# Optimization experiments

Measured on AMD Instinct MI355X. Metric: run time of the kernel, lower is better.

## Reference

```python
import math
import jax, jax.numpy as jnp
import numpy as np
from jax import lax

N_NODES = 325
D = 64
K = 12
E = 2600
SLOTS = 288
WEEK = 7
CHUNK = 24  # 2016 = 84 * 24; chunking does not change the math (disconnected copies)


def _mlp2(x, w1, b1, w2, b2):
    return jax.nn.relu(x @ w1 + b1) @ w2 + b2


def _gru_last_hidden(seq, w_ih, w_hh, b_ih, b_hh, hid):
    # seq: [N, K, 1]; torch nn.GRU gate equations, return final hidden [N, hid]
    def step(h, x_t):
        gi = x_t @ w_ih + b_ih            # [N, 3H]
        gh = h @ w_hh + b_hh
        i_r, i_z, i_n = jnp.split(gi, 3, axis=-1)
        h_r, h_z, h_n = jnp.split(gh, 3, axis=-1)
        r = jax.nn.sigmoid(i_r + h_r)
        z = jax.nn.sigmoid(i_z + h_z)
        n = jnp.tanh(i_n + r * h_n)
        return (1.0 - z) * n + z * h, None
    h0 = jnp.zeros((seq.shape[0], hid), seq.dtype)
    h, _ = lax.scan(step, h0, jnp.swapaxes(seq, 0, 1))  # scan over K
    return h


def _gat(x, src, dst, W, att_src, att_dst, bias, n_nodes):
    # PyG GATConv (self loops already appended to src/dst), concat=False -> head mean
    # x: [C, N, Din]; W: [Din, H*Dh]; att_*: [H, Dh]
    C = x.shape[0]
    H, Dh = att_src.shape
    xp = (x @ W).reshape(C, n_nodes, H, Dh)
    a_s = jnp.sum(xp * att_src, axis=-1)   # [C, N, H]
    a_d = jnp.sum(xp * att_dst, axis=-1)
    e = jax.nn.leaky_relu(a_s[:, src] + a_d[:, dst], 0.2)   # [C, Eb, H]
    seg_max = jax.vmap(lambda v: jax.ops.segment_max(v, dst, num_segments=n_nodes))(e)
    ex = jnp.exp(e - seg_max[:, dst])
    den = jax.vmap(lambda v: jax.ops.segment_sum(v, dst, num_segments=n_nodes))(ex)
    alpha = ex / (den[:, dst] + 1e-16)                       # softmax per dst node
    msg = xp[:, src] * alpha[..., None]                      # [C, Eb, H, Dh]
    out = jax.vmap(lambda m: jax.ops.segment_sum(m, dst, num_segments=n_nodes))(msg)
    return out.mean(axis=2) + bias                           # [C, N, Dh]


def setup_inputs() -> dict:
    key = jax.random.key(0)
    ks = iter(jax.random.split(key, 40))
    s = 0.05
    f = jnp.float32
    p = {}
    p["H_base_bank"] = jax.random.normal(next(ks), (WEEK, SLOTS, N_NODES, D), f)
    p["recent_speed_seq"] = jax.random.normal(next(ks), (N_NODES, K, 1), f)
    p["edge_index"] = jax.random.randint(next(ks), (2, E), 0, N_NODES, jnp.int64 if jax.config.jax_enable_x64 else jnp.int32)
    # GRU (input 1 -> hidden 32)
    p["gru_w_ih"] = jax.random.normal(next(ks), (1, 96), f) * s
    p["gru_w_hh"] = jax.random.normal(next(ks), (32, 96), f) * s
    p["gru_b_ih"] = jnp.zeros((96,), f)
    p["gru_b_hh"] = jnp.zeros((96,), f)
    # recent proj MLP 32->32->32
    p["rp_w1"] = jax.random.normal(next(ks), (32, 32), f) * s; p["rp_b1"] = jnp.zeros((32,), f)
    p["rp_w2"] = jax.random.normal(next(ks), (32, 32), f) * s; p["rp_b2"] = jnp.zeros((32,), f)
    # calendar
    p["weekday_emb"] = jax.random.normal(next(ks), (7, 8), f) * s
    p["slot_emb"] = jax.random.normal(next(ks), (288, 16), f) * s
    p["cal_w1"] = jax.random.normal(next(ks), (29, 32), f) * s; p["cal_b1"] = jnp.zeros((32,), f)
    p["cal_w2"] = jax.random.normal(next(ks), (32, 32), f) * s; p["cal_b2"] = jnp.zeros((32,), f)
    # delta / gate MLPs (fusion 128 -> 64)
    p["dm_w1"] = jax.random.normal(next(ks), (128, 64), f) * s; p["dm_b1"] = jnp.zeros((64,), f)
    p["dm_w2"] = jax.random.normal(next(ks), (64, 64), f) * s;  p["dm_b2"] = jnp.zeros((64,), f)
    p["gm_w"] = jax.random.normal(next(ks), (128, 64), f) * s;  p["gm_b"] = jnp.zeros((64,), f)
    # GATConv 1 (heads=2, concat=False) and 2 (heads=1)
    p["g1_w"] = jax.random.normal(next(ks), (64, 128), f) * s
    p["g1_att_src"] = jax.random.normal(next(ks), (2, 64), f) * s
    p["g1_att_dst"] = jax.random.normal(next(ks), (2, 64), f) * s
    p["g1_bias"] = jnp.zeros((64,), f)
    p["g2_w"] = jax.random.normal(next(ks), (64, 64), f) * s
    p["g2_att_src"] = jax.random.normal(next(ks), (1, 64), f) * s
    p["g2_att_dst"] = jax.random.normal(next(ks), (1, 64), f) * s
    p["g2_bias"] = jnp.zeros((64,), f)
    # speed head 64->32->1
    p["sh_w1"] = jax.random.normal(next(ks), (64, 32), f) * s; p["sh_b1"] = jnp.zeros((32,), f)
    p["sh_w2"] = jax.random.normal(next(ks), (32, 1), f) * s;  p["sh_b2"] = jnp.zeros((1,), f)
    return p


def reference(H_base_bank, recent_speed_seq, edge_index,
              gru_w_ih, gru_w_hh, gru_b_ih, gru_b_hh,
              rp_w1, rp_b1, rp_w2, rp_b2,
              weekday_emb, slot_emb, cal_w1, cal_b1, cal_w2, cal_b2,
              dm_w1, dm_b1, dm_w2, dm_b2, gm_w, gm_b,
              g1_w, g1_att_src, g1_att_dst, g1_bias,
              g2_w, g2_att_src, g2_att_dst, g2_bias,
              sh_w1, sh_b1, sh_w2, sh_b2):
    W_, S_, N, Dm = H_base_bank.shape
    # --- recent encoder ---
    h = _gru_last_hidden(recent_speed_seq, gru_w_ih, gru_w_hh, gru_b_ih, gru_b_hh, 32)
    recent_summary = _mlp2(h, rp_w1, rp_b1, rp_w2, rp_b2)          # [N, 32]
    # --- calendar encoder ---
    w_ids = jnp.repeat(jnp.arange(WEEK)[:, None], SLOTS, axis=1)    # [7, 288]
    s_ids = jnp.repeat(jnp.arange(SLOTS)[None, :], WEEK, axis=0)
    w_e = weekday_emb[w_ids]
    s_e = slot_emb[s_ids]
    ta = 2.0 * math.pi * s_ids.astype(jnp.float32) / 288.0
    wa = 2.0 * math.pi * w_ids.astype(jnp.float32) / 7.0
    cyc = jnp.stack([jnp.sin(ta), jnp.cos(ta), jnp.sin(wa), jnp.cos(wa)], axis=-1)
    wknd = (w_ids >= 5).astype(jnp.float32)[..., None]
    cal_feat = jnp.concatenate([w_e, s_e, cyc, wknd], axis=-1)      # [7, 288, 29]
    calendar_emb = _mlp2(cal_feat, cal_w1, cal_b1, cal_w2, cal_b2)  # [7, 288, 32]
    # --- fusion ---
    rec_x = jnp.broadcast_to(recent_summary[None, None], (W_, S_, N, 32))
    cal_x = jnp.broadcast_to(calendar_emb[:, :, None, :], (W_, S_, N, 32))
    fusion = jnp.concatenate([H_base_bank, rec_x, cal_x], axis=-1)  # [7, 288, N, 128]
    delta_raw = _mlp2(fusion, dm_w1, dm_b1, dm_w2, dm_b2)
    gate = jax.nn.sigmoid(fusion @ gm_w + gm_b)
    delta = delta_raw * gate                                         # [7, 288, N, D]
    # --- graph propagation (GATConv adds self loops by default) ---
    src = jnp.concatenate([edge_index[0], jnp.arange(N, dtype=edge_index.dtype)])
    dst = jnp.concatenate([edge_index[1], jnp.arange(N, dtype=edge_index.dtype)])
    G = W_ * S_
    flat = delta.reshape(G // CHUNK, CHUNK, N, Dm)
    def body(carry, chunk):
        x = jax.nn.relu(_gat(chunk, src, dst, g1_w, g1_att_src, g1_att_dst, g1_bias, N))
        x = jax.nn.relu(_gat(x, src, dst, g2_w, g2_att_src, g2_att_dst, g2_bias, N))
        return carry, x
    _, prop = lax.scan(body, None, flat)
    delta_recent_bank = prop.reshape(W_, S_, N, Dm)
    H_adapted_bank = H_base_bank + delta_recent_bank
    pred_speed_bank = (_mlp2(H_adapted_bank, sh_w1, sh_b1, sh_w2, sh_b2)).squeeze(-1)
    return delta_recent_bank, H_adapted_bank, pred_speed_bank
```

## Files before the change

kernel.cpp:

```cpp
#include <hip/hip_runtime.h>
#include <math.h>

#define N_NODES 325
#define GTOT    2016
#define NPOS    655200
#define NEDGE   2600
#define EBTOT   2925

static __device__ __forceinline__ float bf2f(unsigned short u) {
  union { unsigned int i; float f; } x; x.i = ((unsigned int)u) << 16; return x.f;
}
static __device__ __forceinline__ unsigned short f2bf(float v) {
  union { unsigned int i; float f; } x; x.f = v;
  unsigned int r = x.i + 0x7fffu + ((x.i >> 16) & 1u);
  return (unsigned short)(r >> 16);
}
static __device__ __forceinline__ float sigm(float v) { return 1.f / (1.f + __expf(-v)); }

__global__ void k_csr(const int* __restrict__ ei, int* __restrict__ rowp,
                      int* __restrict__ cols) {
  __shared__ int cnt[N_NODES];
  __shared__ int offs[N_NODES];
  const int tid = threadIdx.x;
  for (int i = tid; i < N_NODES; i += blockDim.x) cnt[i] = 0;
  __syncthreads();
  for (int e = tid; e < EBTOT; e += blockDim.x) {
    int dst = (e < NEDGE) ? ei[NEDGE + e] : (e - NEDGE);
    atomicAdd(&cnt[dst], 1);
  }
  __syncthreads();
  if (tid == 0) {
    int run = 0;
    for (int i = 0; i < N_NODES; ++i) { offs[i] = run; rowp[i] = run; run += cnt[i]; }
    rowp[N_NODES] = run;
  }
  __syncthreads();
  for (int e = tid; e < EBTOT; e += blockDim.x) {
    int src, dst;
    if (e < NEDGE) { src = ei[e]; dst = ei[NEDGE + e]; }
    else           { src = e - NEDGE; dst = src; }
    int pos = atomicAdd(&offs[dst], 1);
    cols[pos] = src;
  }
}

__global__ __launch_bounds__(256) void k_gru(
    const float* __restrict__ seq,
    const float* __restrict__ w_ih, const float* __restrict__ w_hh,
    const float* __restrict__ b_ih, const float* __restrict__ b_hh,
    const float* __restrict__ rw1, const float* __restrict__ rb1,
    const float* __restrict__ rw2, const float* __restrict__ rb2,
    float* __restrict__ recent) {
  __shared__ float h[8][33];
  __shared__ float h2[8][33];
  const int tid = threadIdx.x;
  const int ln = tid >> 5, j = tid & 31;
  const int n = blockIdx.x * 8 + ln;
  h[ln][j] = 0.f;
  __syncthreads();
  for (int t = 0; t < 12; ++t) {
    float x = (n < N_NODES) ? seq[n * 12 + t] : 0.f;
    float i_r = fmaf(x, w_ih[j],      b_ih[j]);
    float i_z = fmaf(x, w_ih[32 + j], b_ih[32 + j]);
    float i_n = fmaf(x, w_ih[64 + j], b_ih[64 + j]);
    float h_r = b_hh[j], h_z = b_hh[32 + j], h_n = b_hh[64 + j];
    #pragma unroll
    for (int k = 0; k < 32; ++k) {
      float hk = h[ln][k];
      h_r = fmaf(hk, w_hh[k * 96 + j],      h_r);
      h_z = fmaf(hk, w_hh[k * 96 + 32 + j], h_z);
      h_n = fmaf(hk, w_hh[k * 96 + 64 + j], h_n);
    }
    float r  = sigm(i_r + h_r);
    float z  = sigm(i_z + h_z);
    float nn = tanhf(fmaf(r, h_n, i_n));
    float hw = (1.f - z) * nn + z * h[ln][j];
    __syncthreads();
    h[ln][j] = hw;
    __syncthreads();
  }
  float a = rb1[j];
  #pragma unroll
  for (int k = 0; k < 32; ++k) a = fmaf(h[ln][k], rw1[k * 32 + j], a);
  h2[ln][j] = fmaxf(a, 0.f);
  __syncthreads();
  float o = rb2[j];
  #pragma unroll
  for (int k = 0; k < 32; ++k) o = fmaf(h2[ln][k], rw2[k * 32 + j], o);
  if (n < N_NODES) recent[n * 32 + j] = o;
}

__global__ __launch_bounds__(256) void k_cal(
    const float* __restrict__ wemb, const float* __restrict__ semb,
    const float* __restrict__ w1, const float* __restrict__ b1,
    const float* __restrict__ w2, const float* __restrict__ b2,
    float* __restrict__ cal) {
  __shared__ float feat[8][32];
  __shared__ float hid[8][33];
  const int tid = threadIdx.x;
  const int ln = tid >> 5, j = tid & 31;
  const int pos = blockIdx.x * 8 + ln;
  const int w = pos / 288, s = pos - w * 288;
  const float TWO_PI = 6.283185307179586f;
  float f = 0.f;
  if (j < 8)       f = wemb[w * 8 + j];
  else if (j < 24) f = semb[s * 16 + (j - 8)];
  else if (j == 24) f = sinf(TWO_PI * (float)s / 288.f);
  else if (j == 25) f = cosf(TWO_PI * (float)s / 288.f);
  else if (j == 26) f = sinf(TWO_PI * (float)w / 7.f);
  else if (j == 27) f = cosf(TWO_PI * (float)w / 7.f);
  else if (j == 28) f = (w >= 5) ? 1.f : 0.f;
  feat[ln][j] = f;
  __syncthreads();
  float a = b1[j];
  #pragma unroll
  for (int k = 0; k < 29; ++k) a = fmaf(feat[ln][k], w1[k * 32 + j], a);
  hid[ln][j] = fmaxf(a, 0.f);
  __syncthreads();
  float o = b2[j];
  #pragma unroll
  for (int k = 0; k < 32; ++k) o = fmaf(hid[ln][k], w2[k * 32 + j], o);
  if (pos < GTOT) cal[pos * 32 + j] = o;
}

__global__ __launch_bounds__(256, 2) void k_fusion(
    const float* __restrict__ Hb, const float* __restrict__ recent,
    const float* __restrict__ cal,
    const float* __restrict__ dw1, const float* __restrict__ db1,
    const float* __restrict__ dw2, const float* __restrict__ db2,
    const float* __restrict__ gw,  const float* __restrict__ gb,
    float* __restrict__ delta) {
  __shared__ float fu[64 * 130];
  __shared__ float hid[64 * 66];
  const int tid = threadIdx.x;
  const int p0 = blockIdx.x * 64;
  for (int idx = tid; idx < 64 * 128; idx += 256) {
    int pl = idx >> 7, k = idx & 127;
    int p = p0 + pl;
    float v = 0.f;
    if (p < NPOS) {
      int g = p / N_NODES;
      int n = p - g * N_NODES;
      if (k < 64)      v = Hb[(size_t)p * 64 + k];
      else if (k < 96) v = recent[n * 32 + (k - 64)];
      else             v = cal[g * 32 + (k - 96)];
    }
    fu[pl * 130 + k] = v;
  }
  __syncthreads();
  const int j0  = (tid & 7) * 8;
  const int pl0 = (tid >> 3) * 2;
  const float* fr0 = fu + pl0 * 130;
  const float* fr1 = fr0 + 130;

  float a0[8], a1[8];
  #pragma unroll
  for (int jj = 0; jj < 8; ++jj) { a0[jj] = db1[j0 + jj]; a1[jj] = a0[jj]; }
  #pragma unroll 2
  for (int k = 0; k < 128; ++k) {
    float4 wa = *(const float4*)(dw1 + k * 64 + j0);
    float4 wb = *(const float4*)(dw1 + k * 64 + j0 + 4);
    float f0 = fr0[k], f1 = fr1[k];
    a0[0]=fmaf(f0,wa.x,a0[0]); a1[0]=fmaf(f1,wa.x,a1[0]);
    a0[1]=fmaf(f0,wa.y,a0[1]); a1[1]=fmaf(f1,wa.y,a1[1]);
    a0[2]=fmaf(f0,wa.z,a0[2]); a1[2]=fmaf(f1,wa.z,a1[2]);
    a0[3]=fmaf(f0,wa.w,a0[3]); a1[3]=fmaf(f1,wa.w,a1[3]);
    a0[4]=fmaf(f0,wb.x,a0[4]); a1[4]=fmaf(f1,wb.x,a1[4]);
    a0[5]=fmaf(f0,wb.y,a0[5]); a1[5]=fmaf(f1,wb.y,a1[5]);
    a0[6]=fmaf(f0,wb.z,a0[6]); a1[6]=fmaf(f1,wb.z,a1[6]);
    a0[7]=fmaf(f0,wb.w,a0[7]); a1[7]=fmaf(f1,wb.w,a1[7]);
  }
  float* hr0 = hid + pl0 * 66;
  float* hr1 = hr0 + 66;
  #pragma unroll
  for (int jj = 0; jj < 8; ++jj) {
    hr0[j0 + jj] = fmaxf(a0[jj], 0.f);
    hr1[j0 + jj] = fmaxf(a1[jj], 0.f);
  }
  __syncthreads();

  float g0[8], g1[8];
  #pragma unroll
  for (int jj = 0; jj < 8; ++jj) { g0[jj] = gb[j0 + jj]; g1[jj] = g0[jj]; }
  #pragma unroll 2
  for (int k = 0; k < 128; ++k) {
    float4 wa = *(const float4*)(gw + k * 64 + j0);
    float4 wb = *(const float4*)(gw + k * 64 + j0 + 4);
    float f0 = fr0[k], f1 = fr1[k];
    g0[0]=fmaf(f0,wa.x,g0[0]); g1[0]=fmaf(f1,wa.x,g1[0]);
    g0[1]=fmaf(f0,wa.y,g0[1]); g1[1]=fmaf(f1,wa.y,g1[1]);
    g0[2]=fmaf(f0,wa.z,g0[2]); g1[2]=fmaf(f1,wa.z,g1[2]);
    g0[3]=fmaf(f0,wa.w,g0[3]); g1[3]=fmaf(f1,wa.w,g1[3]);
    g0[4]=fmaf(f0,wb.x,g0[4]); g1[4]=fmaf(f1,wb.x,g1[4]);
    g0[5]=fmaf(f0,wb.y,g0[5]); g1[5]=fmaf(f1,wb.y,g1[5]);
    g0[6]=fmaf(f0,wb.z,g0[6]); g1[6]=fmaf(f1,wb.z,g1[6]);
    g0[7]=fmaf(f0,wb.w,g0[7]); g1[7]=fmaf(f1,wb.w,g1[7]);
  }
  float d0[8], d1[8];
  #pragma unroll
  for (int jj = 0; jj < 8; ++jj) { d0[jj] = db2[j0 + jj]; d1[jj] = d0[jj]; }
  #pragma unroll 2
  for (int k = 0; k < 64; ++k) {
    float4 wa = *(const float4*)(dw2 + k * 64 + j0);
    float4 wb = *(const float4*)(dw2 + k * 64 + j0 + 4);
    float h0 = hr0[k], h1 = hr1[k];
    d0[0]=fmaf(h0,wa.x,d0[0]); d1[0]=fmaf(h1,wa.x,d1[0]);
    d0[1]=fmaf(h0,wa.y,d0[1]); d1[1]=fmaf(h1,wa.y,d1[1]);
    d0[2]=fmaf(h0,wa.z,d0[2]); d1[2]=fmaf(h1,wa.z,d1[2]);
    d0[3]=fmaf(h0,wa.w,d0[3]); d1[3]=fmaf(h1,wa.w,d1[3]);
    d0[4]=fmaf(h0,wb.x,d0[4]); d1[4]=fmaf(h1,wb.x,d1[4]);
    d0[5]=fmaf(h0,wb.y,d0[5]); d1[5]=fmaf(h1,wb.y,d1[5]);
    d0[6]=fmaf(h0,wb.z,d0[6]); d1[6]=fmaf(h1,wb.z,d1[6]);
    d0[7]=fmaf(h0,wb.w,d0[7]); d1[7]=fmaf(h1,wb.w,d1[7]);
  }
  int pA = p0 + pl0;
  if (pA < NPOS) {
    float4 o;
    o.x=d0[0]*sigm(g0[0]); o.y=d0[1]*sigm(g0[1]); o.z=d0[2]*sigm(g0[2]); o.w=d0[3]*sigm(g0[3]);
    *(float4*)(delta + (size_t)pA * 64 + j0) = o;
    o.x=d0[4]*sigm(g0[4]); o.y=d0[5]*sigm(g0[5]); o.z=d0[6]*sigm(g0[6]); o.w=d0[7]*sigm(g0[7]);
    *(float4*)(delta + (size_t)pA * 64 + j0 + 4) = o;
  }
  if (pA + 1 < NPOS) {
    float4 o;
    o.x=d1[0]*sigm(g1[0]); o.y=d1[1]*sigm(g1[1]); o.z=d1[2]*sigm(g1[2]); o.w=d1[3]*sigm(g1[3]);
    *(float4*)(delta + (size_t)(pA + 1) * 64 + j0) = o;
    o.x=d1[4]*sigm(g1[4]); o.y=d1[5]*sigm(g1[5]); o.z=d1[6]*sigm(g1[6]); o.w=d1[7]*sigm(g1[7]);
    *(float4*)(delta + (size_t)(pA + 1) * 64 + j0 + 4) = o;
  }
}

__global__ __launch_bounds__(256, 3) void k_gat1(
    const float* __restrict__ x,
    const int* __restrict__ rowp, const int* __restrict__ cols,
    const float* __restrict__ W,
    const float* __restrict__ att_s, const float* __restrict__ att_d,
    const float* __restrict__ bias,
    float* __restrict__ y) {
  __shared__ unsigned short xp[N_NODES * 66];
  __shared__ float as_[N_NODES];
  __shared__ float ad_[N_NODES];
  __shared__ unsigned short lw[EBTOT + 3];
  const int tid = threadIdx.x;
  const int lane = tid & 63;
  const int wv = tid >> 6;
  const int c = blockIdx.x;
  const float* xc = x + (size_t)c * (N_NODES * 64);
  float* yc = y + (size_t)c * (N_NODES * 64);
  const float blane = bias[lane];
  for (int h = 0; h < 2; ++h) {
    {
      float wreg[64];
      const float* wcol = W + h * 64 + lane;
      #pragma unroll
      for (int q = 0; q < 64; ++q) wreg[q] = wcol[q * 128];
      const float atts = att_s[h * 64 + lane];
      const float attd = att_d[h * 64 + lane];
      for (int n = wv; n < N_NODES; n += 4) {
        const float4* xr = (const float4*)(xc + n * 64);
        float a0 = 0.f, a1 = 0.f, a2 = 0.f, a3 = 0.f;
        #pragma unroll
        for (int q4 = 0; q4 < 16; ++q4) {
          float4 xv = xr[q4];
          a0 = fmaf(xv.x, wreg[4 * q4 + 0], a0);
          a1 = fmaf(xv.y, wreg[4 * q4 + 1], a1);
          a2 = fmaf(xv.z, wreg[4 * q4 + 2], a2);
          a3 = fmaf(xv.w, wreg[4 * q4 + 3], a3);
        }
        float acc = (a0 + a1) + (a2 + a3);
        xp[n * 66 + lane] = f2bf(acc);
        float ps = acc * atts, pd = acc * attd;
        #pragma unroll
        for (int off = 32; off; off >>= 1) {
          ps += __shfl_xor(ps, off);
          pd += __shfl_xor(pd, off);
        }
        if (lane == 0) { as_[n] = ps; ad_[n] = pd; }
      }
    }
    __syncthreads();
    for (int d = tid; d < N_NODES; d += 256) {
      int rb = rowp[d], re = rowp[d + 1];
      float adv = ad_[d];
      for (int e = rb; e < re; ++e) {
        float v = as_[cols[e]] + adv;
        lw[e] = f2bf((v >= 0.f) ? v : 0.2f * v);
      }
    }
    __syncthreads();
    for (int d = wv; d < N_NODES; d += 4) {
      int rb = __builtin_amdgcn_readfirstlane(rowp[d]);
      int re = __builtin_amdgcn_readfirstlane(rowp[d + 1]);
      float prev = (h == 1) ? yc[d * 64 + lane] : 0.f;
      float dn0 = 0.f, dn1 = 0.f, dn2 = 0.f, dn3 = 0.f;
      float ac0 = 0.f, ac1 = 0.f, ac2 = 0.f, ac3 = 0.f;
      for (int e0 = rb; e0 < re; e0 += 4) {
        int e1 = e0 + 1, e2 = e0 + 2, e3 = e0 + 3;
        bool k1 = e1 < re, k2 = e2 < re, k3 = e3 < re;
        int s0 = cols[e0];
        int s1 = cols[k1 ? e1 : e0];
        int s2 = cols[k2 ? e2 : e0];
        int s3 = cols[k3 ? e3 : e0];
        float w0 = __expf(bf2f(lw[e0]));
        float w1 = k1 ? __expf(bf2f(lw[e1])) : 0.f;
        float w2 = k2 ? __expf(bf2f(lw[e2])) : 0.f;
        float w3 = k3 ? __expf(bf2f(lw[e3])) : 0.f;
        dn0 += w0; dn1 += w1; dn2 += w2; dn3 += w3;
        ac0 = fmaf(w0, bf2f(xp[s0 * 66 + lane]), ac0);
        ac1 = fmaf(w1, bf2f(xp[s1 * 66 + lane]), ac1);
        ac2 = fmaf(w2, bf2f(xp[s2 * 66 + lane]), ac2);
        ac3 = fmaf(w3, bf2f(xp[s3 * 66 + lane]), ac3);
      }
      float den = (dn0 + dn1) + (dn2 + dn3);
      float acc = (ac0 + ac1) + (ac2 + ac3);
      float o = acc / (den + 1e-16f);
      if (h == 0) {
        yc[d * 64 + lane] = o;
      } else {
        yc[d * 64 + lane] = fmaxf(0.5f * (prev + o) + blane, 0.f);
      }
    }
    __syncthreads();
  }
}

__global__ __launch_bounds__(256, 3) void k_gat2(
    const float* x,
    const float* __restrict__ Hb,
    const int* __restrict__ rowp, const int* __restrict__ cols,
    const float* __restrict__ W,
    const float* __restrict__ att_s, const float* __restrict__ att_d,
    const float* __restrict__ bias,
    const float* __restrict__ shw1, const float* __restrict__ shb1,
    const float* __restrict__ shw2, const float* __restrict__ shb2,
    float* dR, float* __restrict__ Ha, float* __restrict__ pred) {
  __shared__ unsigned short xp[N_NODES * 66];
  __shared__ float as_[N_NODES];
  __shared__ float ad_[N_NODES];
  __shared__ unsigned short lw[EBTOT + 3];
  __shared__ float hv[4][68];
  const int tid = threadIdx.x;
  const int lane = tid & 63;
  const int wv = tid >> 6;
  const int c = blockIdx.x;
  const float* xc = x + (size_t)c * (N_NODES * 64);
  const float blane = bias[lane];
  {
    float wreg[64];
    const float* wcol = W + lane;
    #pragma unroll
    for (int q = 0; q < 64; ++q) wreg[q] = wcol[q * 64];
    const float atts = att_s[lane];
    const float attd = att_d[lane];
    for (int n = wv; n < N_NODES; n += 4) {
      const float4* xr = (const float4*)(xc + n * 64);
      float a0 = 0.f, a1 = 0.f, a2 = 0.f, a3 = 0.f;
      #pragma unroll
      for (int q4 = 0; q4 < 16; ++q4) {
        float4 xv = xr[q4];
        a0 = fmaf(xv.x, wreg[4 * q4 + 0], a0);
        a1 = fmaf(xv.y, wreg[4 * q4 + 1], a1);
        a2 = fmaf(xv.z, wreg[4 * q4 + 2], a2);
        a3 = fmaf(xv.w, wreg[4 * q4 + 3], a3);
      }
      float acc = (a0 + a1) + (a2 + a3);
      xp[n * 66 + lane] = f2bf(acc);
      float ps = acc * atts, pd = acc * attd;
      #pragma unroll
      for (int off = 32; off; off >>= 1) {
        ps += __shfl_xor(ps, off);
        pd += __shfl_xor(pd, off);
      }
      if (lane == 0) { as_[n] = ps; ad_[n] = pd; }
    }
  }
  __syncthreads();
  for (int d = tid; d < N_NODES; d += 256) {
    int rb = rowp[d], re = rowp[d + 1];
    float adv = ad_[d];
    for (int e = rb; e < re; ++e) {
      float v = as_[cols[e]] + adv;
      lw[e] = f2bf((v >= 0.f) ? v : 0.2f * v);
    }
  }
  __syncthreads();
  const int j = lane & 31, qh = lane >> 5;
  float sw1r[32];
  #pragma unroll
  for (int q = 0; q < 32; ++q) sw1r[q] = shw1[(qh * 32 + q) * 32 + j];
  const float sw2r = shw2[j];
  const float sb1r = shb1[j];
  const float sb2  = shb2[0];
  for (int d = wv; d < N_NODES; d += 4) {
    int rb = __builtin_amdgcn_readfirstlane(rowp[d]);
    int re = __builtin_amdgcn_readfirstlane(rowp[d + 1]);
    size_t base = (size_t)c * (N_NODES * 64) + (size_t)d * 64 + lane;
    float hbv = Hb[base];
    float dn0 = 0.f, dn1 = 0.f, dn2 = 0.f, dn3 = 0.f;
    float ac0 = 0.f, ac1 = 0.f, ac2 = 0.f, ac3 = 0.f;
    for (int e0 = rb; e0 < re; e0 += 4) {
      int e1 = e0 + 1, e2 = e0 + 2, e3 = e0 + 3;
      bool k1 = e1 < re, k2 = e2 < re, k3 = e3 < re;
      int s0 = cols[e0];
      int s1 = cols[k1 ? e1 : e0];
      int s2 = cols[k2 ? e2 : e0];
      int s3 = cols[k3 ? e3 : e0];
      float w0 = __expf(bf2f(lw[e0]));
      float w1 = k1 ? __expf(bf2f(lw[e1])) : 0.f;
      float w2 = k2 ? __expf(bf2f(lw[e2])) : 0.f;
      float w3 = k3 ? __expf(bf2f(lw[e3])) : 0.f;
      dn0 += w0; dn1 += w1; dn2 += w2; dn3 += w3;
      ac0 = fmaf(w0, bf2f(xp[s0 * 66 + lane]), ac0);
      ac1 = fmaf(w1, bf2f(xp[s1 * 66 + lane]), ac1);
      ac2 = fmaf(w2, bf2f(xp[s2 * 66 + lane]), ac2);
      ac3 = fmaf(w3, bf2f(xp[s3 * 66 + lane]), ac3);
    }
    float den = (dn0 + dn1) + (dn2 + dn3);
    float acc = (ac0 + ac1) + (ac2 + ac3);
    float val = fmaxf(acc / (den + 1e-16f) + blane, 0.f);
    dR[base] = val;
    float had = hbv + val;
    Ha[base] = had;
    hv[wv][lane] = had;
    float p0 = 0.f, p1 = 0.f, p2 = 0.f, p3 = 0.f;
    const float* hrow = &hv[wv][qh * 32];
    #pragma unroll
    for (int q = 0; q < 32; q += 4) {
      p0 = fmaf(hrow[q + 0], sw1r[q + 0], p0);
      p1 = fmaf(hrow[q + 1], sw1r[q + 1], p1);
      p2 = fmaf(hrow[q + 2], sw1r[q + 2], p2);
      p3 = fmaf(hrow[q + 3], sw1r[q + 3], p3);
    }
    float a = (p0 + p1) + (p2 + p3);
    a += __shfl_xor(a, 32);
    a = fmaxf(a + sb1r, 0.f) * sw2r;
    #pragma unroll
    for (int off = 16; off; off >>= 1) a += __shfl_xor(a, off);
    if (lane == 0) pred[c * N_NODES + d] = a + sb2;
  }
}

extern "C" void kernel_launch(void* const* d_in, const int* in_sizes, int n_in,
                              void* d_out, int out_size, void* d_ws, size_t ws_size,
                              hipStream_t stream) {
  const float* Hb    = (const float*)d_in[0];
  const float* seq   = (const float*)d_in[1];
  const int*   ei    = (const int*)d_in[2];
  const float* gwih  = (const float*)d_in[3];
  const float* gwhh  = (const float*)d_in[4];
  const float* gbih  = (const float*)d_in[5];
  const float* gbhh  = (const float*)d_in[6];
  const float* rw1   = (const float*)d_in[7];
  const float* rb1   = (const float*)d_in[8];
  const float* rw2   = (const float*)d_in[9];
  const float* rb2   = (const float*)d_in[10];
  const float* wemb  = (const float*)d_in[11];
  const float* semb  = (const float*)d_in[12];
  const float* cw1   = (const float*)d_in[13];
  const float* cb1   = (const float*)d_in[14];
  const float* cw2   = (const float*)d_in[15];
  const float* cb2   = (const float*)d_in[16];
  const float* dw1   = (const float*)d_in[17];
  const float* db1   = (const float*)d_in[18];
  const float* dw2   = (const float*)d_in[19];
  const float* db2   = (const float*)d_in[20];
  const float* gmw   = (const float*)d_in[21];
  const float* gmb   = (const float*)d_in[22];
  const float* g1w   = (const float*)d_in[23];
  const float* g1as  = (const float*)d_in[24];
  const float* g1ad  = (const float*)d_in[25];
  const float* g1b   = (const float*)d_in[26];
  const float* g2w   = (const float*)d_in[27];
  const float* g2as  = (const float*)d_in[28];
  const float* g2ad  = (const float*)d_in[29];
  const float* g2b   = (const float*)d_in[30];
  const float* shw1  = (const float*)d_in[31];
  const float* shb1  = (const float*)d_in[32];
  const float* shw2  = (const float*)d_in[33];
  const float* shb2  = (const float*)d_in[34];

  float* out = (float*)d_out;
  float* region0 = out;
  float* region1 = out + 41932800u;
  float* region2 = out + 83865600u;

  float* delta = region1;
  float* y1    = region0;

  int* rowp = (int*)d_ws;
  int* cols = rowp + 384;
  float* recent = (float*)(rowp + 3328);
  float* cal    = recent + 10400;

  k_csr<<<1, 512, 0, stream>>>(ei, rowp, cols);
  k_gru<<<(N_NODES + 7) / 8, 256, 0, stream>>>(seq, gwih, gwhh, gbih, gbhh,
                                               rw1, rb1, rw2, rb2, recent);
  k_cal<<<GTOT / 8, 256, 0, stream>>>(wemb, semb, cw1, cb1, cw2, cb2, cal);
  k_fusion<<<(NPOS + 63) / 64, 256, 0, stream>>>(Hb, recent, cal,
                                                 dw1, db1, dw2, db2, gmw, gmb, delta);
  k_gat1<<<GTOT, 256, 0, stream>>>(delta, rowp, cols, g1w, g1as, g1ad, g1b, y1);
  k_gat2<<<GTOT, 256, 0, stream>>>(y1, Hb, rowp, cols, g2w, g2as, g2ad, g2b,
                                   shw1, shb1, shw2, shb2,
                                   region0, region1, region2);
}
```

Baseline: 3.226 ms.

## Widen GAT blocks to 512 threads, pair node projections, split attention-score pass

Both GAT kernels now launch 512 threads (8 waves) per graph chunk, and each wave projects two nodes per iteration so one set of register weights serves two rows. The attention-score dot products move out of the projection loop into a separate per-node pass that reads the bf16 projected features from shared memory, which removes the per-node cross-lane shuffle reductions. Launch bounds also change for k_fusion (2 to 3 blocks) and the GAT kernels (512,4). The gains sought are more latency hiding and fewer shuffles. The costs are an extra barrier, attention scores computed from bf16-rounded values, and register pressure that may force spills under the tighter bounds.

```diff
diff --git a/kernel.cpp b/kernel.cpp
--- a/kernel.cpp
+++ b/kernel.cpp
@@ -123,7 +123,7 @@
   if (pos < GTOT) cal[pos * 32 + j] = o;
 }
 
-__global__ __launch_bounds__(256, 2) void k_fusion(
+__global__ __launch_bounds__(256, 3) void k_fusion(
     const float* __restrict__ Hb, const float* __restrict__ recent,
     const float* __restrict__ cal,
     const float* __restrict__ dw1, const float* __restrict__ db1,
@@ -230,7 +230,7 @@
   }
 }
 
-__global__ __launch_bounds__(256, 3) void k_gat1(
+__global__ __launch_bounds__(512, 4) void k_gat1(
     const float* __restrict__ x,
     const int* __restrict__ rowp, const int* __restrict__ cols,
     const float* __restrict__ W,
@@ -254,32 +254,51 @@
       const float* wcol = W + h * 64 + lane;
       #pragma unroll
       for (int q = 0; q < 64; ++q) wreg[q] = wcol[q * 128];
-      const float atts = att_s[h * 64 + lane];
-      const float attd = att_d[h * 64 + lane];
-      for (int n = wv; n < N_NODES; n += 4) {
-        const float4* xr = (const float4*)(xc + n * 64);
-        float a0 = 0.f, a1 = 0.f, a2 = 0.f, a3 = 0.f;
+      for (int n0 = wv * 2; n0 < N_NODES; n0 += 16) {
+        const int n1 = n0 + 1;
+        const bool has1 = (n1 < N_NODES);
+        const float4* xr0 = (const float4*)(xc + n0 * 64);
+        const float4* xr1 = (const float4*)(xc + (has1 ? n1 : n0) * 64);
+        float a0 = 0.f, a1 = 0.f, b0 = 0.f, b1 = 0.f;
         #pragma unroll
         for (int q4 = 0; q4 < 16; ++q4) {
-          float4 xv = xr[q4];
-          a0 = fmaf(xv.x, wreg[4 * q4 + 0], a0);
-          a1 = fmaf(xv.y, wreg[4 * q4 + 1], a1);
-          a2 = fmaf(xv.z, wreg[4 * q4 + 2], a2);
-          a3 = fmaf(xv.w, wreg[4 * q4 + 3], a3);
+          float4 xv0 = xr0[q4];
+          float4 xv1 = xr1[q4];
+          a0 = fmaf(xv0.x, wreg[4 * q4 + 0], a0);
+          a1 = fmaf(xv0.y, wreg[4 * q4 + 1], a1);
+          a0 = fmaf(xv0.z, wreg[4 * q4 + 2], a0);
+          a1 = fmaf(xv0.w, wreg[4 * q4 + 3], a1);
+          b0 = fmaf(xv1.x, wreg[4 * q4 + 0], b0);
+          b1 = fmaf(xv1.y, wreg[4 * q4 + 1], b1);
+          b0 = fmaf(xv1.z, wreg[4 * q4 + 2], b0);
+          b1 = fmaf(xv1.w, wreg[4 * q4 + 3], b1);
         }
-        float acc = (a0 + a1) + (a2 + a3);
-        xp[n * 66 + lane] = f2bf(acc);
-        float ps = acc * atts, pd = acc * attd;
+        xp[n0 * 66 + lane] = f2bf(a0 + a1);
+        if (has1) xp[n1 * 66 + lane] = f2bf(b0 + b1);
+      }
+    }
+    __syncthreads();
+    {
+      const float* aw_s = att_s + h * 64;
+      const float* aw_d = att_d + h * 64;
+      for (int n = tid; n < N_NODES; n += 512) {
+        const unsigned short* xr = xp + n * 66;
+        float s0 = 0.f, s1 = 0.f, d0 = 0.f, d1 = 0.f;
         #pragma unroll
-        for (int off = 32; off; off >>= 1) {
-          ps += __shfl_xor(ps, off);
-          pd += __shfl_xor(pd, off);
+        for (int k = 0; k < 64; k += 2) {
+          float v0 = bf2f(xr[k]);
+          float v1 = bf2f(xr[k + 1]);
+          s0 = fmaf(v0, aw_s[k],     s0);
+          d0 = fmaf(v0, aw_d[k],     d0);
+          s1 = fmaf(v1, aw_s[k + 1], s1);
+          d1 = fmaf(v1, aw_d[k + 1], d1);
         }
-        if (lane == 0) { as_[n] = ps; ad_[n] = pd; }
+        as_[n] = s0 + s1;
+        ad_[n] = d0 + d1;
       }
     }
     __syncthreads();
-    for (int d = tid; d < N_NODES; d += 256) {
+    for (int d = tid; d < N_NODES; d += 512) {
       int rb = rowp[d], re = rowp[d + 1];
       float adv = ad_[d];
       for (int e = rb; e < re; ++e) {
@@ -288,7 +307,7 @@
       }
     }
     __syncthreads();
-    for (int d = wv; d < N_NODES; d += 4) {
+    for (int d = wv; d < N_NODES; d += 8) {
       int rb = __builtin_amdgcn_readfirstlane(rowp[d]);
       int re = __builtin_amdgcn_readfirstlane(rowp[d + 1]);
       float prev = (h == 1) ? yc[d * 64 + lane] : 0.f;
@@ -324,7 +343,7 @@
   }
 }
 
-__global__ __launch_bounds__(256, 3) void k_gat2(
+__global__ __launch_bounds__(512, 4) void k_gat2(
     const float* x,
     const float* __restrict__ Hb,
     const int* __restrict__ rowp, const int* __restrict__ cols,
@@ -338,7 +357,7 @@
   __shared__ float as_[N_NODES];
   __shared__ float ad_[N_NODES];
   __shared__ unsigned short lw[EBTOT + 3];
-  __shared__ float hv[4][68];
+  __shared__ float hv[8][68];
   const int tid = threadIdx.x;
   const int lane = tid & 63;
   const int wv = tid >> 6;
@@ -350,32 +369,47 @@
     const float* wcol = W + lane;
     #pragma unroll
     for (int q = 0; q < 64; ++q) wreg[q] = wcol[q * 64];
-    const float atts = att_s[lane];
-    const float attd = att_d[lane];
-    for (int n = wv; n < N_NODES; n += 4) {
-      const float4* xr = (const float4*)(xc + n * 64);
-      float a0 = 0.f, a1 = 0.f, a2 = 0.f, a3 = 0.f;
+    for (int n0 = wv * 2; n0 < N_NODES; n0 += 16) {
+      const int n1 = n0 + 1;
+      const bool has1 = (n1 < N_NODES);
+      const float4* xr0 = (const float4*)(xc + n0 * 64);
+      const float4* xr1 = (const float4*)(xc + (has1 ? n1 : n0) * 64);
+      float a0 = 0.f, a1 = 0.f, b0 = 0.f, b1 = 0.f;
       #pragma unroll
       for (int q4 = 0; q4 < 16; ++q4) {
-        float4 xv = xr[q4];
-        a0 = fmaf(xv.x, wreg[4 * q4 + 0], a0);
-        a1 = fmaf(xv.y, wreg[4 * q4 + 1], a1);
-        a2 = fmaf(xv.z, wreg[4 * q4 + 2], a2);
-        a3 = fmaf(xv.w, wreg[4 * q4 + 3], a3);
+        float4 xv0 = xr0[q4];
+        float4 xv1 = xr1[q4];
+        a0 = fmaf(xv0.x, wreg[4 * q4 + 0], a0);
+        a1 = fmaf(xv0.y, wreg[4 * q4 + 1], a1);
+        a0 = fmaf(xv0.z, wreg[4 * q4 + 2], a0);
+        a1 = fmaf(xv0.w, wreg[4 * q4 + 3], a1);
+        b0 = fmaf(xv1.x, wreg[4 * q4 + 0], b0);
+        b1 = fmaf(xv1.y, wreg[4 * q4 + 1], b1);
+        b0 = fmaf(xv1.z, wreg[4 * q4 + 2], b0);
+        b1 = fmaf(xv1.w, wreg[4 * q4 + 3], b1);
       }
-      float acc = (a0 + a1) + (a2 + a3);
-      xp[n * 66 + lane] = f2bf(acc);
-      float ps = acc * atts, pd = acc * attd;
-      #pragma unroll
-      for (int off = 32; off; off >>= 1) {
-        ps += __shfl_xor(ps, off);
-        pd += __shfl_xor(pd, off);
-      }
-      if (lane == 0) { as_[n] = ps; ad_[n] = pd; }
-    }
-  }
-  __syncthreads();
-  for (int d = tid; d < N_NODES; d += 256) {
+      xp[n0 * 66 + lane] = f2bf(a0 + a1);
+      if (has1) xp[n1 * 66 + lane] = f2bf(b0 + b1);
+    }
+  }
+  __syncthreads();
+  for (int n = tid; n < N_NODES; n += 512) {
+    const unsigned short* xr = xp + n * 66;
+    float s0 = 0.f, s1 = 0.f, d0 = 0.f, d1 = 0.f;
+    #pragma unroll
+    for (int k = 0; k < 64; k += 2) {
+      float v0 = bf2f(xr[k]);
+      float v1 = bf2f(xr[k + 1]);
+      s0 = fmaf(v0, att_s[k],     s0);
+      d0 = fmaf(v0, att_d[k],     d0);
+      s1 = fmaf(v1, att_s[k + 1], s1);
+      d1 = fmaf(v1, att_d[k + 1], d1);
+    }
+    as_[n] = s0 + s1;
+    ad_[n] = d0 + d1;
+  }
+  __syncthreads();
+  for (int d = tid; d < N_NODES; d += 512) {
     int rb = rowp[d], re = rowp[d + 1];
     float adv = ad_[d];
     for (int e = rb; e < re; ++e) {
@@ -391,7 +425,7 @@
   const float sw2r = shw2[j];
   const float sb1r = shb1[j];
   const float sb2  = shb2[0];
-  for (int d = wv; d < N_NODES; d += 4) {
+  for (int d = wv; d < N_NODES; d += 8) {
     int rb = __builtin_amdgcn_readfirstlane(rowp[d]);
     int re = __builtin_amdgcn_readfirstlane(rowp[d + 1]);
     size_t base = (size_t)c * (N_NODES * 64) + (size_t)d * 64 + lane;
@@ -498,8 +532,8 @@
   k_cal<<<GTOT / 8, 256, 0, stream>>>(wemb, semb, cw1, cb1, cw2, cb2, cal);
   k_fusion<<<(NPOS + 63) / 64, 256, 0, stream>>>(Hb, recent, cal,
                                                  dw1, db1, dw2, db2, gmw, gmb, delta);
-  k_gat1<<<GTOT, 256, 0, stream>>>(delta, rowp, cols, g1w, g1as, g1ad, g1b, y1);
-  k_gat2<<<GTOT, 256, 0, stream>>>(y1, Hb, rowp, cols, g2w, g2as, g2ad, g2b,
+  k_gat1<<<GTOT, 512, 0, stream>>>(delta, rowp, cols, g1w, g1as, g1ad, g1b, y1);
+  k_gat2<<<GTOT, 512, 0, stream>>>(y1, Hb, rowp, cols, g2w, g2as, g2ad, g2b,
                                    shw1, shb1, shw2, shb2,
                                    region0, region1, region2);
 }
```

Result: slower. 9.798 ms (+203.7%).
